# Performance work log

Measured on AMD Instinct MI355X. Metric: run time of the kernel, lower is better.

The kernel has to match this reference:

```python
import jax, jax.numpy as jnp
import numpy as np

D = 1024
N_HEADS = 16
D_HEAD = D // N_HEADS


def setup_inputs() -> dict:
    key = jax.random.key(0)
    ks = jax.random.split(key, 7)
    B, S = 4, 1024
    x = jax.random.normal(ks[0], (B, S, D), dtype=jnp.float32)
    # per-head linear params, stacked over heads: W[h] is [d_head, d_head] (torch Linear weight),
    # y = s @ W[h].T + b[h]
    scale = 1.0 / np.sqrt(D_HEAD)
    Wq = jax.random.uniform(ks[1], (N_HEADS, D_HEAD, D_HEAD), jnp.float32, -scale, scale)
    Wk = jax.random.uniform(ks[2], (N_HEADS, D_HEAD, D_HEAD), jnp.float32, -scale, scale)
    Wv = jax.random.uniform(ks[3], (N_HEADS, D_HEAD, D_HEAD), jnp.float32, -scale, scale)
    bq = jax.random.uniform(ks[4], (N_HEADS, D_HEAD), jnp.float32, -scale, scale)
    bk = jax.random.uniform(ks[5], (N_HEADS, D_HEAD), jnp.float32, -scale, scale)
    bv = jax.random.uniform(ks[6], (N_HEADS, D_HEAD), jnp.float32, -scale, scale)
    return {"pix_sequences": x, "Wq": Wq, "Wk": Wk, "Wv": Wv,
            "bq": bq, "bk": bk, "bv": bv}


def reference(pix_sequences, Wq, Wk, Wv, bq, bk, bv):
    B, S, d = pix_sequences.shape
    # split feature dim into heads: [B, S, H, dh]
    xh = pix_sequences.reshape(B, S, N_HEADS, D_HEAD)
    # per-head linear: y = s @ W.T + b
    q = jnp.einsum('bshd,hed->bshe', xh, Wq) + bq  # [B,S,H,dh]
    k = jnp.einsum('bshd,hed->bshe', xh, Wk) + bk
    v = jnp.einsum('bshd,hed->bshe', xh, Wv) + bv
    scores = jnp.einsum('bqhd,bkhd->bhqk', q, k) / jnp.sqrt(jnp.float32(D_HEAD))
    attn = jax.nn.softmax(scores, axis=-1)  # [B,H,S,S]
    out = jnp.einsum('bhqk,bkhd->bqhd', attn, v)  # [B,S,H,dh]
    return out.reshape(B, S, d)
```

## Files before the change

kernel.cpp:

```cpp
#include <hip/hip_runtime.h>
#include <hip/hip_bf16.h>

constexpr int BB = 4;
constexpr int SS = 1024;
constexpr int HH = 16;
constexpr int DH = 64;
constexpr int DM = 1024;

using f32x16 = __attribute__((ext_vector_type(16))) float;
using s16x8  = __attribute__((ext_vector_type(8))) short;

__device__ __forceinline__ f32x16 mfma32(s16x8 a, s16x8 b, f32x16 c) {
    return __builtin_amdgcn_mfma_f32_32x32x16_bf16(a, b, c, 0, 0, 0);
}

__device__ __forceinline__ unsigned short bf16bits(float x) {
    union { __hip_bfloat16 h; unsigned short s; } cv;
    cv.h = __float2bfloat16(x);
    return cv.s;
}
__device__ __forceinline__ unsigned pk_bf16(float lo, float hi) {
    return (unsigned)bf16bits(lo) | ((unsigned)bf16bits(hi) << 16);
}

__device__ __forceinline__ float fast_exp2(float x) {
#if __has_builtin(__builtin_amdgcn_exp2f)
    return __builtin_amdgcn_exp2f(x);
#else
    return __expf(x * 0.6931471805599453f);
#endif
}

__global__ __launch_bounds__(256) void qkv_proj_kernel(
    const float* __restrict__ x,
    const float* __restrict__ Wq, const float* __restrict__ Wk, const float* __restrict__ Wv,
    const float* __restrict__ bq, const float* __restrict__ bk, const float* __restrict__ bv,
    __hip_bfloat16* __restrict__ q_ws, __hip_bfloat16* __restrict__ k_ws,
    __hip_bfloat16* __restrict__ v_ws)
{
    const int bid  = blockIdx.x;
    const int tile = bid & 7;
    const int pair = bid >> 3;
    const int b = pair >> 4, h = pair & 15;
    const int t = threadIdx.x;
    const int w = t >> 6, l = t & 63;
    const int lq = l & 31, hi = l >> 5;
    const int s0 = tile * 128;

    __shared__ __align__(16) char Xs[16384];
    __shared__ __align__(16) char Kt[16384];
    __shared__ __align__(16) char Vt[16384];

    {
        const float* xb = x + (size_t)(b * SS + s0) * DM + h * DH;
        #pragma unroll
        for (int i = 0; i < 8; ++i) {
            const int c  = t + 256 * i;
            const int r  = c >> 4, cw = c & 15;
            float4 v4 = *reinterpret_cast<const float4*>(xb + (size_t)r * DM + cw * 4);
            uint2 p;
            p.x = pk_bf16(v4.x, v4.y);
            p.y = pk_bf16(v4.z, v4.w);
            *reinterpret_cast<uint2*>(Xs + r * 128 + ((cw * 8) ^ ((r & 7) << 4))) = p;
        }
    }
    __syncthreads();

    const int arow = w * 32 + lq;
    const int asw  = (arow & 7) << 4;
    s16x8 af[4];
    #pragma unroll
    for (int s = 0; s < 4; ++s)
        af[s] = *reinterpret_cast<const s16x8*>(Xs + arow * 128 + ((s * 32 + hi * 16) ^ asw));
    __syncthreads();

    #pragma unroll
    for (int m = 0; m < 3; ++m) {
        const float* Wm = (m == 0) ? Wq : (m == 1) ? Wk : Wv;
        const float* bm = (m == 0) ? bq : (m == 1) ? bk : bv;

        f32x16 a0, a1;
        #pragma unroll
        for (int r = 0; r < 16; ++r) { a0[r] = 0.0f; a1[r] = 0.0f; }

        #pragma unroll
        for (int s = 0; s < 4; ++s) {
            const float* wp0 = Wm + (size_t)(h * DH + lq) * DH + s * 16 + hi * 8;
            const float* wp1 = wp0 + 32 * DH;
            float4 wa0 = reinterpret_cast<const float4*>(wp0)[0];
            float4 wb0 = reinterpret_cast<const float4*>(wp0)[1];
            float4 wa1 = reinterpret_cast<const float4*>(wp1)[0];
            float4 wb1 = reinterpret_cast<const float4*>(wp1)[1];
            union { unsigned u[4]; s16x8 v; } bf0, bf1;
            bf0.u[0] = pk_bf16(wa0.x, wa0.y); bf0.u[1] = pk_bf16(wa0.z, wa0.w);
            bf0.u[2] = pk_bf16(wb0.x, wb0.y); bf0.u[3] = pk_bf16(wb0.z, wb0.w);
            bf1.u[0] = pk_bf16(wa1.x, wa1.y); bf1.u[1] = pk_bf16(wa1.z, wa1.w);
            bf1.u[2] = pk_bf16(wb1.x, wb1.y); bf1.u[3] = pk_bf16(wb1.z, wb1.w);
            a0 = mfma32(af[s], bf0.v, a0);
            a1 = mfma32(af[s], bf1.v, a1);
        }

        const float bias0 = bm[h * DH + lq];
        const float bias1 = bm[h * DH + 32 + lq];

        if (m < 2) {
            char* T = (m == 0) ? Xs : Kt;
            #pragma unroll
            for (int r = 0; r < 16; ++r) {
                const int row = w * 32 + (r & 3) + 8 * (r >> 2) + 4 * hi;
                const int sw  = (row & 7) << 4;
                *reinterpret_cast<unsigned short*>(T + row * 128 + ((lq * 2) ^ sw)) =
                    bf16bits(a0[r] + bias0);
                *reinterpret_cast<unsigned short*>(T + row * 128 + (((32 + lq) * 2) ^ sw)) =
                    bf16bits(a1[r] + bias1);
            }
        } else {
            #pragma unroll
            for (int g = 0; g < 4; ++g) {
                const int off = w * 64 + g * 16 + hi * 8;
                uint2 p0, p1;
                p0.x = pk_bf16(a0[4*g+0] + bias0, a0[4*g+1] + bias0);
                p0.y = pk_bf16(a0[4*g+2] + bias0, a0[4*g+3] + bias0);
                p1.x = pk_bf16(a1[4*g+0] + bias1, a1[4*g+1] + bias1);
                p1.y = pk_bf16(a1[4*g+2] + bias1, a1[4*g+3] + bias1);
                *reinterpret_cast<uint2*>(Vt + lq * 256 + (off ^ ((lq & 7) << 4))) = p0;
                *reinterpret_cast<uint2*>(Vt + (32 + lq) * 256 + (off ^ (((32 + lq) & 7) << 4))) = p1;
            }
        }
    }
    __syncthreads();

    #pragma unroll
    for (int i = 0; i < 4; ++i) {
        const int c   = t + 256 * i;
        const int row = c >> 3, cc = c & 7;
        const int off = row * 128 + ((cc * 16) ^ ((row & 7) << 4));
        s16x8 qv = *reinterpret_cast<const s16x8*>(Xs + off);
        *reinterpret_cast<s16x8*>(q_ws + ((size_t)pair * SS + s0 + row) * DH + cc * 8) = qv;
        s16x8 kv = *reinterpret_cast<const s16x8*>(Kt + off);
        *reinterpret_cast<s16x8*>(k_ws + ((size_t)pair * SS + s0 + row) * DH + cc * 8) = kv;
    }
    #pragma unroll
    for (int i = 0; i < 4; ++i) {
        const int c   = t + 256 * i;
        const int row = c >> 4, cc = c & 15;
        s16x8 vv = *reinterpret_cast<const s16x8*>(
            Vt + row * 256 + ((cc * 16) ^ ((row & 7) << 4)));
        *reinterpret_cast<s16x8*>(v_ws + ((size_t)pair * DH + row) * SS + s0 + cc * 8) = vv;
    }
}

__global__ __launch_bounds__(256) void attn_kernel(
    const __hip_bfloat16* __restrict__ q_ws,
    const __hip_bfloat16* __restrict__ k_ws,
    const __hip_bfloat16* __restrict__ v_ws,
    float* __restrict__ out)
{
    const int bid  = blockIdx.x;
    const int lbid = (bid & 7) * 64 + (bid >> 3);
    const int qt   = lbid & 7;
    const int pair = lbid >> 3;
    const int b = pair >> 4, h = pair & 15;
    const int t = threadIdx.x;
    const int w = t >> 6, l = t & 63;
    const int lq = l & 31, hi = l >> 5;

    __shared__ __align__(16) char Kl[2][8192];
    __shared__ __align__(16) char Vl[2][8192];

    const __hip_bfloat16* qp = q_ws + ((size_t)pair * SS + qt * 128 + w * 32 + lq) * DH + hi * 8;
    s16x8 qf[4];
    #pragma unroll
    for (int s5 = 0; s5 < 4; ++s5)
        qf[s5] = *reinterpret_cast<const s16x8*>(qp + s5 * 16);

    const int u0 = t, u1 = t + 256;
    const __hip_bfloat16* kb = k_ws + (size_t)pair * SS * DH;
    const __hip_bfloat16* vb = v_ws + (size_t)pair * DH * SS;
    const int ksw0 = (u0 ^ ((u0 >> 3) & 7)) * 16;
    const int ksw1 = (u1 ^ ((u1 >> 3) & 7)) * 16;
    const size_t voff0 = (size_t)(u0 >> 3) * SS + (u0 & 7) * 8;
    const size_t voff1 = (size_t)(u1 >> 3) * SS + (u1 & 7) * 8;

    {
        s16x8 k0 = *reinterpret_cast<const s16x8*>(kb + u0 * 8);
        s16x8 k1 = *reinterpret_cast<const s16x8*>(kb + u1 * 8);
        s16x8 v0 = *reinterpret_cast<const s16x8*>(vb + voff0);
        s16x8 v1 = *reinterpret_cast<const s16x8*>(vb + voff1);
        *reinterpret_cast<s16x8*>(Kl[0] + ksw0) = k0;
        *reinterpret_cast<s16x8*>(Kl[0] + ksw1) = k1;
        *reinterpret_cast<s16x8*>(Vl[0] + ksw0) = v0;
        *reinterpret_cast<s16x8*>(Vl[0] + ksw1) = v1;
    }
    __syncthreads();

    f32x16 o0, o1;
    #pragma unroll
    for (int r = 0; r < 16; ++r) { o0[r] = 0.0f; o1[r] = 0.0f; }
    float m_run = -3.0e38f, lsum = 0.0f;
    const float cml = 0.18033688011112042f;

    const int kbase0 = lq * 128;
    const int kbase1 = (32 + lq) * 128;
    const int swz = (lq & 7) << 4;

    int p = 0;
    s16x8 kr0, kr1, vr0, vr1;
    for (int kt = 0; kt < 16; ++kt) {
        if (kt < 15) {
            kr0 = *reinterpret_cast<const s16x8*>(kb + (kt + 1) * 4096 + u0 * 8);
            kr1 = *reinterpret_cast<const s16x8*>(kb + (kt + 1) * 4096 + u1 * 8);
            vr0 = *reinterpret_cast<const s16x8*>(vb + voff0 + (kt + 1) * 64);
            vr1 = *reinterpret_cast<const s16x8*>(vb + voff1 + (kt + 1) * 64);
        }
        const char* Kp = Kl[p];
        const char* Vp = Vl[p];

        f32x16 sc0, sc1;
        #pragma unroll
        for (int r = 0; r < 16; ++r) { sc0[r] = 0.0f; sc1[r] = 0.0f; }
        #pragma unroll
        for (int s5 = 0; s5 < 4; ++s5) {
            const int co = (2 * s5 + hi) << 4;
            s16x8 ka = *reinterpret_cast<const s16x8*>(Kp + kbase0 + (co ^ swz));
            sc0 = mfma32(ka, qf[s5], sc0);
        }
        #pragma unroll
        for (int s5 = 0; s5 < 4; ++s5) {
            const int co = (2 * s5 + hi) << 4;
            s16x8 ka = *reinterpret_cast<const s16x8*>(Kp + kbase1 + (co ^ swz));
            sc1 = mfma32(ka, qf[s5], sc1);
        }

        float tm[16];
        #pragma unroll
        for (int r = 0; r < 16; ++r) tm[r] = fmaxf(sc0[r], sc1[r]);
        #pragma unroll
        for (int s = 8; s >= 1; s >>= 1)
            #pragma unroll
            for (int r = 0; r < 8; ++r)
                if (r < s) tm[r] = fmaxf(tm[r], tm[r + s]);
        float mx = fmaxf(tm[0], __shfl_xor(tm[0], 32));

        if (!__all((mx - m_run) * cml <= 8.0f)) {
            float mnew  = fmaxf(m_run, mx);
            float alpha = fast_exp2((m_run - mnew) * cml);
            lsum *= alpha;
            #pragma unroll
            for (int r = 0; r < 16; ++r) { o0[r] *= alpha; o1[r] *= alpha; }
            m_run = mnew;
        }
        const float nm = -m_run * cml;
        float ts[16];
        #pragma unroll
        for (int r = 0; r < 16; ++r) {
            sc0[r] = fast_exp2(fmaf(sc0[r], cml, nm));
            sc1[r] = fast_exp2(fmaf(sc1[r], cml, nm));
            ts[r]  = sc0[r] + sc1[r];
        }
        #pragma unroll
        for (int s = 8; s >= 1; s >>= 1)
            #pragma unroll
            for (int r = 0; r < 8; ++r)
                if (r < s) ts[r] += ts[r + s];
        lsum += ts[0] + __shfl_xor(ts[0], 32);

        #pragma unroll
        for (int s5 = 0; s5 < 4; ++s5) {
            const int sb8 = (s5 & 1) * 8;
            unsigned a0, b0, a1, b1;
            if (s5 < 2) {
                a0 = pk_bf16(sc0[sb8 + 0], sc0[sb8 + 1]);
                b0 = pk_bf16(sc0[sb8 + 4], sc0[sb8 + 5]);
                a1 = pk_bf16(sc0[sb8 + 2], sc0[sb8 + 3]);
                b1 = pk_bf16(sc0[sb8 + 6], sc0[sb8 + 7]);
            } else {
                a0 = pk_bf16(sc1[sb8 + 0], sc1[sb8 + 1]);
                b0 = pk_bf16(sc1[sb8 + 4], sc1[sb8 + 5]);
                a1 = pk_bf16(sc1[sb8 + 2], sc1[sb8 + 3]);
                b1 = pk_bf16(sc1[sb8 + 6], sc1[sb8 + 7]);
            }
            const unsigned sa0 = (unsigned)__shfl_xor((int)a0, 32);
            const unsigned sb0 = (unsigned)__shfl_xor((int)b0, 32);
            const unsigned sa1 = (unsigned)__shfl_xor((int)a1, 32);
            const unsigned sb1 = (unsigned)__shfl_xor((int)b1, 32);
            union { unsigned u[4]; s16x8 v; } afr;
            afr.u[0] = hi ? sb0 : a0;
            afr.u[1] = hi ? sb1 : a1;
            afr.u[2] = hi ? b0 : sa0;
            afr.u[3] = hi ? b1 : sa1;
            const int co = (2 * s5 + hi) << 4;
            s16x8 vb0 = *reinterpret_cast<const s16x8*>(Vp + kbase0 + (co ^ swz));
            o0 = mfma32(afr.v, vb0, o0);
            s16x8 vb1 = *reinterpret_cast<const s16x8*>(Vp + kbase1 + (co ^ swz));
            o1 = mfma32(afr.v, vb1, o1);
        }

        if (kt < 15) {
            *reinterpret_cast<s16x8*>(Kl[p ^ 1] + ksw0) = kr0;
            *reinterpret_cast<s16x8*>(Kl[p ^ 1] + ksw1) = kr1;
            *reinterpret_cast<s16x8*>(Vl[p ^ 1] + ksw0) = vr0;
            *reinterpret_cast<s16x8*>(Vl[p ^ 1] + ksw1) = vr1;
        }
        __syncthreads();
        p ^= 1;
    }

    const float inv = 1.0f / lsum;
    #pragma unroll
    for (int r = 0; r < 16; ++r) {
        const int qr = (r & 3) + 8 * (r >> 2) + 4 * hi;
        const float invr = __shfl(inv, qr);
        float* op = out + ((size_t)b * SS + qt * 128 + w * 32 + qr) * DM + h * DH + lq;
        op[0]  = o0[r] * invr;
        op[32] = o1[r] * invr;
    }
}

extern "C" void kernel_launch(void* const* d_in, const int* in_sizes, int n_in,
                              void* d_out, int out_size, void* d_ws, size_t ws_size,
                              hipStream_t stream) {
    const float* x  = (const float*)d_in[0];
    const float* Wq = (const float*)d_in[1];
    const float* Wk = (const float*)d_in[2];
    const float* Wv = (const float*)d_in[3];
    const float* bq = (const float*)d_in[4];
    const float* bk = (const float*)d_in[5];
    const float* bv = (const float*)d_in[6];
    float* out = (float*)d_out;

    __hip_bfloat16* q_ws = (__hip_bfloat16*)d_ws;
    __hip_bfloat16* k_ws = q_ws + (size_t)BB * HH * SS * DH;
    __hip_bfloat16* v_ws = k_ws + (size_t)BB * HH * SS * DH;

    qkv_proj_kernel<<<dim3(BB * HH * (SS / 128)), dim3(256), 0, stream>>>(
        x, Wq, Wk, Wv, bq, bk, bv, q_ws, k_ws, v_ws);
    attn_kernel<<<dim3(BB * HH * (SS / 64 / 2)), dim3(256), 0, stream>>>(
        q_ws, k_ws, v_ws, out);
}
```

Measured before the change: 60.02 us.

## Split KV range across two warp groups per block and merge softmax partials

```diff
diff --git a/kernel.cpp b/kernel.cpp
--- a/kernel.cpp
+++ b/kernel.cpp
@@ -150,7 +150,7 @@
     }
 }
 
-__global__ __launch_bounds__(256) void attn_kernel(
+__global__ __launch_bounds__(512, 4) void attn_kernel(
     const __hip_bfloat16* __restrict__ q_ws,
     const __hip_bfloat16* __restrict__ k_ws,
     const __hip_bfloat16* __restrict__ v_ws,
@@ -164,33 +164,36 @@
     const int t = threadIdx.x;
     const int w = t >> 6, l = t & 63;
     const int lq = l & 31, hi = l >> 5;
-
-    __shared__ __align__(16) char Kl[2][8192];
-    __shared__ __align__(16) char Vl[2][8192];
-
-    const __hip_bfloat16* qp = q_ws + ((size_t)pair * SS + qt * 128 + w * 32 + lq) * DH + hi * 8;
+    const int qg = w & 3, p = w >> 2;
+
+    __shared__ __align__(16) char smem[65536];
+
+    const __hip_bfloat16* qp =
+        q_ws + ((size_t)pair * SS + qt * 128 + qg * 32 + lq) * DH + hi * 8;
     s16x8 qf[4];
     #pragma unroll
     for (int s5 = 0; s5 < 4; ++s5)
         qf[s5] = *reinterpret_cast<const s16x8*>(qp + s5 * 16);
 
-    const int u0 = t, u1 = t + 256;
+    const int u0 = t, u1 = t + 512;
     const __hip_bfloat16* kb = k_ws + (size_t)pair * SS * DH;
     const __hip_bfloat16* vb = v_ws + (size_t)pair * DH * SS;
-    const int ksw0 = (u0 ^ ((u0 >> 3) & 7)) * 16;
-    const int ksw1 = (u1 ^ ((u1 >> 3) & 7)) * 16;
-    const size_t voff0 = (size_t)(u0 >> 3) * SS + (u0 & 7) * 8;
-    const size_t voff1 = (size_t)(u1 >> 3) * SS + (u1 & 7) * 8;
+    const int kOff0 = (u0 ^ ((u0 >> 3) & 7)) * 16;
+    const int kOff1 = (u1 ^ ((u1 >> 3) & 7)) * 16;
+    const int vOff0 = (u0 >> 4) * 256 + (((u0 & 15) ^ ((u0 >> 4) & 15)) << 4);
+    const int vOff1 = (u1 >> 4) * 256 + (((u1 & 15) ^ ((u1 >> 4) & 15)) << 4);
+    const size_t vs0 = (size_t)(u0 >> 4) * SS + (u0 & 15) * 8;
+    const size_t vs1 = (size_t)(u1 >> 4) * SS + (u1 & 15) * 8;
 
     {
         s16x8 k0 = *reinterpret_cast<const s16x8*>(kb + u0 * 8);
         s16x8 k1 = *reinterpret_cast<const s16x8*>(kb + u1 * 8);
-        s16x8 v0 = *reinterpret_cast<const s16x8*>(vb + voff0);
-        s16x8 v1 = *reinterpret_cast<const s16x8*>(vb + voff1);
-        *reinterpret_cast<s16x8*>(Kl[0] + ksw0) = k0;
-        *reinterpret_cast<s16x8*>(Kl[0] + ksw1) = k1;
-        *reinterpret_cast<s16x8*>(Vl[0] + ksw0) = v0;
-        *reinterpret_cast<s16x8*>(Vl[0] + ksw1) = v1;
+        s16x8 v0 = *reinterpret_cast<const s16x8*>(vb + vs0);
+        s16x8 v1 = *reinterpret_cast<const s16x8*>(vb + vs1);
+        *reinterpret_cast<s16x8*>(smem + kOff0) = k0;
+        *reinterpret_cast<s16x8*>(smem + kOff1) = k1;
+        *reinterpret_cast<s16x8*>(smem + 16384 + vOff0) = v0;
+        *reinterpret_cast<s16x8*>(smem + 16384 + vOff1) = v1;
     }
     __syncthreads();
 
@@ -200,21 +203,23 @@
     float m_run = -3.0e38f, lsum = 0.0f;
     const float cml = 0.18033688011112042f;
 
-    const int kbase0 = lq * 128;
-    const int kbase1 = (32 + lq) * 128;
-    const int swz = (lq & 7) << 4;
-
-    int p = 0;
+    const int kbase0 = (p * 64 + lq) * 128;
+    const int kbase1 = kbase0 + 32 * 128;
+    const int swzK = (lq & 7) << 4;
+    const int swzV = (lq & 15) << 4;
+    const int vrow0 = lq * 256, vrow1 = (32 + lq) * 256;
+
+    int bufp = 0;
     s16x8 kr0, kr1, vr0, vr1;
-    for (int kt = 0; kt < 16; ++kt) {
-        if (kt < 15) {
-            kr0 = *reinterpret_cast<const s16x8*>(kb + (kt + 1) * 4096 + u0 * 8);
-            kr1 = *reinterpret_cast<const s16x8*>(kb + (kt + 1) * 4096 + u1 * 8);
-            vr0 = *reinterpret_cast<const s16x8*>(vb + voff0 + (kt + 1) * 64);
-            vr1 = *reinterpret_cast<const s16x8*>(vb + voff1 + (kt + 1) * 64);
-        }
-        const char* Kp = Kl[p];
-        const char* Vp = Vl[p];
+    for (int st = 0; st < 8; ++st) {
+        if (st < 7) {
+            kr0 = *reinterpret_cast<const s16x8*>(kb + (st + 1) * 8192 + u0 * 8);
+            kr1 = *reinterpret_cast<const s16x8*>(kb + (st + 1) * 8192 + u1 * 8);
+            vr0 = *reinterpret_cast<const s16x8*>(vb + vs0 + (st + 1) * 128);
+            vr1 = *reinterpret_cast<const s16x8*>(vb + vs1 + (st + 1) * 128);
+        }
+        const char* Kp = smem + bufp * 32768;
+        const char* Vp = Kp + 16384;
 
         f32x16 sc0, sc1;
         #pragma unroll
@@ -222,13 +227,13 @@
         #pragma unroll
         for (int s5 = 0; s5 < 4; ++s5) {
             const int co = (2 * s5 + hi) << 4;
-            s16x8 ka = *reinterpret_cast<const s16x8*>(Kp + kbase0 + (co ^ swz));
+            s16x8 ka = *reinterpret_cast<const s16x8*>(Kp + kbase0 + (co ^ swzK));
             sc0 = mfma32(ka, qf[s5], sc0);
         }
         #pragma unroll
         for (int s5 = 0; s5 < 4; ++s5) {
             const int co = (2 * s5 + hi) << 4;
-            s16x8 ka = *reinterpret_cast<const s16x8*>(Kp + kbase1 + (co ^ swz));
+            s16x8 ka = *reinterpret_cast<const s16x8*>(Kp + kbase1 + (co ^ swzK));
             sc1 = mfma32(ka, qf[s5], sc1);
         }
 
@@ -290,30 +295,53 @@
             afr.u[2] = hi ? b0 : sa0;
             afr.u[3] = hi ? b1 : sa1;
             const int co = (2 * s5 + hi) << 4;
-            s16x8 vb0 = *reinterpret_cast<const s16x8*>(Vp + kbase0 + (co ^ swz));
+            s16x8 vb0 = *reinterpret_cast<const s16x8*>(Vp + vrow0 + ((p * 128 + co) ^ swzV));
             o0 = mfma32(afr.v, vb0, o0);
-            s16x8 vb1 = *reinterpret_cast<const s16x8*>(Vp + kbase1 + (co ^ swz));
+            s16x8 vb1 = *reinterpret_cast<const s16x8*>(Vp + vrow1 + ((p * 128 + co) ^ swzV));
             o1 = mfma32(afr.v, vb1, o1);
         }
 
-        if (kt < 15) {
-            *reinterpret_cast<s16x8*>(Kl[p ^ 1] + ksw0) = kr0;
-            *reinterpret_cast<s16x8*>(Kl[p ^ 1] + ksw1) = kr1;
-            *reinterpret_cast<s16x8*>(Vl[p ^ 1] + ksw0) = vr0;
-            *reinterpret_cast<s16x8*>(Vl[p ^ 1] + ksw1) = vr1;
+        if (st < 7) {
+            char* Kn = smem + (bufp ^ 1) * 32768;
+            *reinterpret_cast<s16x8*>(Kn + kOff0) = kr0;
+            *reinterpret_cast<s16x8*>(Kn + kOff1) = kr1;
+            *reinterpret_cast<s16x8*>(Kn + 16384 + vOff0) = vr0;
+            *reinterpret_cast<s16x8*>(Kn + 16384 + vOff1) = vr1;
         }
         __syncthreads();
-        p ^= 1;
-    }
-
-    const float inv = 1.0f / lsum;
-    #pragma unroll
-    for (int r = 0; r < 16; ++r) {
-        const int qr = (r & 3) + 8 * (r >> 2) + 4 * hi;
-        const float invr = __shfl(inv, qr);
-        float* op = out + ((size_t)b * SS + qt * 128 + w * 32 + qr) * DM + h * DH + lq;
-        op[0]  = o0[r] * invr;
-        op[32] = o1[r] * invr;
+        bufp ^= 1;
+    }
+
+    float* Obuf = reinterpret_cast<float*>(smem + qg * 8192);
+    float* mlb  = reinterpret_cast<float*>(smem + 32768 + qg * 256);
+    if (p == 1) {
+        #pragma unroll
+        for (int r = 0; r < 16; ++r) {
+            const int qr = (r & 3) + 8 * (r >> 2) + 4 * hi;
+            Obuf[qr * 64 + lq]      = o0[r];
+            Obuf[qr * 64 + 32 + lq] = o1[r];
+        }
+        mlb[lq]      = m_run;
+        mlb[32 + lq] = lsum;
+    }
+    __syncthreads();
+    if (p == 0) {
+        const float m1 = mlb[lq];
+        const float l1 = mlb[32 + lq];
+        const float M  = fmaxf(m_run, m1);
+        const float e0 = fast_exp2((m_run - M) * cml);
+        const float e1 = fast_exp2((m1 - M) * cml);
+        const float inv = 1.0f / fmaf(lsum, e0, l1 * e1);
+        const float f0 = e0 * inv, f1 = e1 * inv;
+        #pragma unroll
+        for (int r = 0; r < 16; ++r) {
+            const int qr = (r & 3) + 8 * (r >> 2) + 4 * hi;
+            const float f0r = __shfl(f0, qr);
+            const float f1r = __shfl(f1, qr);
+            float* op = out + ((size_t)b * SS + qt * 128 + qg * 32 + qr) * DM + h * DH + lq;
+            op[0]  = o0[r] * f0r + Obuf[qr * 64 + lq]      * f1r;
+            op[32] = o1[r] * f0r + Obuf[qr * 64 + 32 + lq] * f1r;
+        }
     }
 }
 
@@ -335,6 +363,6 @@
 
     qkv_proj_kernel<<<dim3(BB * HH * (SS / 128)), dim3(256), 0, stream>>>(
         x, Wq, Wk, Wv, bq, bk, bv, q_ws, k_ws, v_ws);
-    attn_kernel<<<dim3(BB * HH * (SS / 64 / 2)), dim3(256), 0, stream>>>(
+    attn_kernel<<<dim3(BB * HH * (SS / 128)), dim3(512), 0, stream>>>(
         q_ws, k_ws, v_ws, out);
 }
```

Measured after the change: 61.39 us. 2.3% more time.

## Split attention KV range across waves with in-block LSE merge

Applied to the files above, without the earlier changes.

```diff
diff --git a/kernel.cpp b/kernel.cpp
--- a/kernel.cpp
+++ b/kernel.cpp
@@ -29,6 +29,11 @@
 #else
     return __expf(x * 0.6931471805599453f);
 #endif
+}
+
+__device__ __forceinline__ int kperm(int g) {
+    const int m = g & 12;
+    return (m == 4 || m == 8) ? (g ^ 12) : g;
 }
 
 __global__ __launch_bounds__(256) void qkv_proj_kernel(
@@ -150,49 +155,32 @@
     }
 }
 
-__global__ __launch_bounds__(256) void attn_kernel(
+__global__ __launch_bounds__(256, 4) void attn_kernel(
     const __hip_bfloat16* __restrict__ q_ws,
     const __hip_bfloat16* __restrict__ k_ws,
     const __hip_bfloat16* __restrict__ v_ws,
     float* __restrict__ out)
 {
     const int bid  = blockIdx.x;
-    const int lbid = (bid & 7) * 64 + (bid >> 3);
-    const int qt   = lbid & 7;
-    const int pair = lbid >> 3;
+    const int lbid = (bid & 7) * 256 + (bid >> 3);
+    const int qg   = lbid & 31;
+    const int pair = lbid >> 5;
     const int b = pair >> 4, h = pair & 15;
     const int t = threadIdx.x;
-    const int w = t >> 6, l = t & 63;
+    const int p = t >> 6, l = t & 63;
     const int lq = l & 31, hi = l >> 5;
 
-    __shared__ __align__(16) char Kl[2][8192];
-    __shared__ __align__(16) char Vl[2][8192];
-
-    const __hip_bfloat16* qp = q_ws + ((size_t)pair * SS + qt * 128 + w * 32 + lq) * DH + hi * 8;
+    __shared__ __align__(16) char smem[16896];
+
+    const __hip_bfloat16* qp = q_ws + ((size_t)pair * SS + qg * 32 + lq) * DH + hi * 8;
     s16x8 qf[4];
     #pragma unroll
     for (int s5 = 0; s5 < 4; ++s5)
         qf[s5] = *reinterpret_cast<const s16x8*>(qp + s5 * 16);
 
-    const int u0 = t, u1 = t + 256;
-    const __hip_bfloat16* kb = k_ws + (size_t)pair * SS * DH;
-    const __hip_bfloat16* vb = v_ws + (size_t)pair * DH * SS;
-    const int ksw0 = (u0 ^ ((u0 >> 3) & 7)) * 16;
-    const int ksw1 = (u1 ^ ((u1 >> 3) & 7)) * 16;
-    const size_t voff0 = (size_t)(u0 >> 3) * SS + (u0 & 7) * 8;
-    const size_t voff1 = (size_t)(u1 >> 3) * SS + (u1 & 7) * 8;
-
-    {
-        s16x8 k0 = *reinterpret_cast<const s16x8*>(kb + u0 * 8);
-        s16x8 k1 = *reinterpret_cast<const s16x8*>(kb + u1 * 8);
-        s16x8 v0 = *reinterpret_cast<const s16x8*>(vb + voff0);
-        s16x8 v1 = *reinterpret_cast<const s16x8*>(vb + voff1);
-        *reinterpret_cast<s16x8*>(Kl[0] + ksw0) = k0;
-        *reinterpret_cast<s16x8*>(Kl[0] + ksw1) = k1;
-        *reinterpret_cast<s16x8*>(Vl[0] + ksw0) = v0;
-        *reinterpret_cast<s16x8*>(Vl[0] + ksw1) = v1;
-    }
-    __syncthreads();
+    const __hip_bfloat16* kp  = k_ws + ((size_t)pair * SS + kperm(lq)) * DH + hi * 8;
+    const __hip_bfloat16* vp0 = v_ws + ((size_t)pair * DH + lq) * SS + hi * 8;
+    const __hip_bfloat16* vp1 = vp0 + (size_t)32 * SS;
 
     f32x16 o0, o1;
     #pragma unroll
@@ -200,41 +188,22 @@
     float m_run = -3.0e38f, lsum = 0.0f;
     const float cml = 0.18033688011112042f;
 
-    const int kbase0 = lq * 128;
-    const int kbase1 = (32 + lq) * 128;
-    const int swz = (lq & 7) << 4;
-
-    int p = 0;
-    s16x8 kr0, kr1, vr0, vr1;
-    for (int kt = 0; kt < 16; ++kt) {
-        if (kt < 15) {
-            kr0 = *reinterpret_cast<const s16x8*>(kb + (kt + 1) * 4096 + u0 * 8);
-            kr1 = *reinterpret_cast<const s16x8*>(kb + (kt + 1) * 4096 + u1 * 8);
-            vr0 = *reinterpret_cast<const s16x8*>(vb + voff0 + (kt + 1) * 64);
-            vr1 = *reinterpret_cast<const s16x8*>(vb + voff1 + (kt + 1) * 64);
-        }
-        const char* Kp = Kl[p];
-        const char* Vp = Vl[p];
-
-        f32x16 sc0, sc1;
-        #pragma unroll
-        for (int r = 0; r < 16; ++r) { sc0[r] = 0.0f; sc1[r] = 0.0f; }
-        #pragma unroll
-        for (int s5 = 0; s5 < 4; ++s5) {
-            const int co = (2 * s5 + hi) << 4;
-            s16x8 ka = *reinterpret_cast<const s16x8*>(Kp + kbase0 + (co ^ swz));
-            sc0 = mfma32(ka, qf[s5], sc0);
-        }
-        #pragma unroll
-        for (int s5 = 0; s5 < 4; ++s5) {
-            const int co = (2 * s5 + hi) << 4;
-            s16x8 ka = *reinterpret_cast<const s16x8*>(Kp + kbase1 + (co ^ swz));
-            sc1 = mfma32(ka, qf[s5], sc1);
-        }
+    for (int g8 = 0; g8 < 8; ++g8) {
+        const int g = p * 8 + g8;
+        const __hip_bfloat16* kg  = kp  + (size_t)g * 32 * DH;
+        const __hip_bfloat16* vg0 = vp0 + g * 32;
+        const __hip_bfloat16* vg1 = vp1 + g * 32;
+
+        f32x16 sc;
+        #pragma unroll
+        for (int r = 0; r < 16; ++r) sc[r] = 0.0f;
+        #pragma unroll
+        for (int s5 = 0; s5 < 4; ++s5)
+            sc = mfma32(*reinterpret_cast<const s16x8*>(kg + s5 * 16), qf[s5], sc);
 
         float tm[16];
         #pragma unroll
-        for (int r = 0; r < 16; ++r) tm[r] = fmaxf(sc0[r], sc1[r]);
+        for (int r = 0; r < 16; ++r) tm[r] = sc[r];
         #pragma unroll
         for (int s = 8; s >= 1; s >>= 1)
             #pragma unroll
@@ -247,16 +216,19 @@
             float alpha = fast_exp2((m_run - mnew) * cml);
             lsum *= alpha;
             #pragma unroll
-            for (int r = 0; r < 16; ++r) { o0[r] *= alpha; o1[r] *= alpha; }
+            for (int r = 0; r < 16; ++r) {
+                const int qr = (r & 3) + 8 * (r >> 2) + 4 * hi;
+                const float ar = __shfl(alpha, qr);
+                o0[r] *= ar; o1[r] *= ar;
+            }
             m_run = mnew;
         }
         const float nm = -m_run * cml;
         float ts[16];
         #pragma unroll
         for (int r = 0; r < 16; ++r) {
-            sc0[r] = fast_exp2(fmaf(sc0[r], cml, nm));
-            sc1[r] = fast_exp2(fmaf(sc1[r], cml, nm));
-            ts[r]  = sc0[r] + sc1[r];
+            sc[r] = fast_exp2(fmaf(sc[r], cml, nm));
+            ts[r] = sc[r];
         }
         #pragma unroll
         for (int s = 8; s >= 1; s >>= 1)
@@ -265,55 +237,84 @@
                 if (r < s) ts[r] += ts[r + s];
         lsum += ts[0] + __shfl_xor(ts[0], 32);
 
-        #pragma unroll
-        for (int s5 = 0; s5 < 4; ++s5) {
-            const int sb8 = (s5 & 1) * 8;
-            unsigned a0, b0, a1, b1;
-            if (s5 < 2) {
-                a0 = pk_bf16(sc0[sb8 + 0], sc0[sb8 + 1]);
-                b0 = pk_bf16(sc0[sb8 + 4], sc0[sb8 + 5]);
-                a1 = pk_bf16(sc0[sb8 + 2], sc0[sb8 + 3]);
-                b1 = pk_bf16(sc0[sb8 + 6], sc0[sb8 + 7]);
-            } else {
-                a0 = pk_bf16(sc1[sb8 + 0], sc1[sb8 + 1]);
-                b0 = pk_bf16(sc1[sb8 + 4], sc1[sb8 + 5]);
-                a1 = pk_bf16(sc1[sb8 + 2], sc1[sb8 + 3]);
-                b1 = pk_bf16(sc1[sb8 + 6], sc1[sb8 + 7]);
-            }
-            const unsigned sa0 = (unsigned)__shfl_xor((int)a0, 32);
-            const unsigned sb0 = (unsigned)__shfl_xor((int)b0, 32);
-            const unsigned sa1 = (unsigned)__shfl_xor((int)a1, 32);
-            const unsigned sb1 = (unsigned)__shfl_xor((int)b1, 32);
-            union { unsigned u[4]; s16x8 v; } afr;
-            afr.u[0] = hi ? sb0 : a0;
-            afr.u[1] = hi ? sb1 : a1;
-            afr.u[2] = hi ? b0 : sa0;
-            afr.u[3] = hi ? b1 : sa1;
-            const int co = (2 * s5 + hi) << 4;
-            s16x8 vb0 = *reinterpret_cast<const s16x8*>(Vp + kbase0 + (co ^ swz));
-            o0 = mfma32(afr.v, vb0, o0);
-            s16x8 vb1 = *reinterpret_cast<const s16x8*>(Vp + kbase1 + (co ^ swz));
-            o1 = mfma32(afr.v, vb1, o1);
-        }
-
-        if (kt < 15) {
-            *reinterpret_cast<s16x8*>(Kl[p ^ 1] + ksw0) = kr0;
-            *reinterpret_cast<s16x8*>(Kl[p ^ 1] + ksw1) = kr1;
-            *reinterpret_cast<s16x8*>(Vl[p ^ 1] + ksw0) = vr0;
-            *reinterpret_cast<s16x8*>(Vl[p ^ 1] + ksw1) = vr1;
-        }
-        __syncthreads();
-        p ^= 1;
-    }
-
-    const float inv = 1.0f / lsum;
-    #pragma unroll
-    for (int r = 0; r < 16; ++r) {
-        const int qr = (r & 3) + 8 * (r >> 2) + 4 * hi;
-        const float invr = __shfl(inv, qr);
-        float* op = out + ((size_t)b * SS + qt * 128 + w * 32 + qr) * DM + h * DH + lq;
-        op[0]  = o0[r] * invr;
-        op[32] = o1[r] * invr;
+        union { unsigned u[4]; s16x8 v; } af0, af1;
+        af0.u[0] = pk_bf16(sc[0], sc[1]);   af0.u[1] = pk_bf16(sc[2], sc[3]);
+        af0.u[2] = pk_bf16(sc[4], sc[5]);   af0.u[3] = pk_bf16(sc[6], sc[7]);
+        af1.u[0] = pk_bf16(sc[8], sc[9]);   af1.u[1] = pk_bf16(sc[10], sc[11]);
+        af1.u[2] = pk_bf16(sc[12], sc[13]); af1.u[3] = pk_bf16(sc[14], sc[15]);
+
+        s16x8 v00 = *reinterpret_cast<const s16x8*>(vg0);
+        s16x8 v01 = *reinterpret_cast<const s16x8*>(vg0 + 16);
+        s16x8 v10 = *reinterpret_cast<const s16x8*>(vg1);
+        s16x8 v11 = *reinterpret_cast<const s16x8*>(vg1 + 16);
+        o0 = mfma32(af0.v, v00, o0);
+        o0 = mfma32(af1.v, v01, o0);
+        o1 = mfma32(af0.v, v10, o1);
+        o1 = mfma32(af1.v, v11, o1);
+    }
+
+    float* O0 = reinterpret_cast<float*>(smem);
+    float* M0 = reinterpret_cast<float*>(smem + 8192);
+    float* O1 = reinterpret_cast<float*>(smem + 8448);
+    float* M1 = reinterpret_cast<float*>(smem + 16640);
+
+    if (p == 1 || p == 3) {
+        float* O = (p == 1) ? O0 : O1;
+        float* M = (p == 1) ? M0 : M1;
+        #pragma unroll
+        for (int r = 0; r < 16; ++r) {
+            const int qr = (r & 3) + 8 * (r >> 2) + 4 * hi;
+            O[qr * 64 + lq]      = o0[r];
+            O[qr * 64 + 32 + lq] = o1[r];
+        }
+        if (hi == 0) { M[lq] = m_run; M[32 + lq] = lsum; }
+    }
+    __syncthreads();
+    if (p == 0 || p == 2) {
+        float* O = (p == 0) ? O0 : O1;
+        float* M = (p == 0) ? M0 : M1;
+        const float m1 = M[lq], l1 = M[32 + lq];
+        const float Mx = fmaxf(m_run, m1);
+        const float e0 = fast_exp2((m_run - Mx) * cml);
+        const float e1 = fast_exp2((m1 - Mx) * cml);
+        #pragma unroll
+        for (int r = 0; r < 16; ++r) {
+            const int qr = (r & 3) + 8 * (r >> 2) + 4 * hi;
+            const float e0r = __shfl(e0, qr);
+            const float e1r = __shfl(e1, qr);
+            o0[r] = o0[r] * e0r + O[qr * 64 + lq] * e1r;
+            o1[r] = o1[r] * e0r + O[qr * 64 + 32 + lq] * e1r;
+        }
+        lsum = lsum * e0 + l1 * e1;
+        m_run = Mx;
+    }
+    __syncthreads();
+    if (p == 2) {
+        #pragma unroll
+        for (int r = 0; r < 16; ++r) {
+            const int qr = (r & 3) + 8 * (r >> 2) + 4 * hi;
+            O1[qr * 64 + lq]      = o0[r];
+            O1[qr * 64 + 32 + lq] = o1[r];
+        }
+        if (hi == 0) { M1[lq] = m_run; M1[32 + lq] = lsum; }
+    }
+    __syncthreads();
+    if (p == 0) {
+        const float m1 = M1[lq], l1 = M1[32 + lq];
+        const float Mx = fmaxf(m_run, m1);
+        const float e0 = fast_exp2((m_run - Mx) * cml);
+        const float e1 = fast_exp2((m1 - Mx) * cml);
+        const float inv = 1.0f / (lsum * e0 + l1 * e1);
+        const float f0 = e0 * inv, f1 = e1 * inv;
+        #pragma unroll
+        for (int r = 0; r < 16; ++r) {
+            const int qr = (r & 3) + 8 * (r >> 2) + 4 * hi;
+            const float f0r = __shfl(f0, qr);
+            const float f1r = __shfl(f1, qr);
+            float* op = out + ((size_t)b * SS + qg * 32 + qr) * DM + h * DH + lq;
+            op[0]  = o0[r] * f0r + O1[qr * 64 + lq]      * f1r;
+            op[32] = o1[r] * f0r + O1[qr * 64 + 32 + lq] * f1r;
+        }
     }
 }
 
@@ -335,6 +336,6 @@
 
     qkv_proj_kernel<<<dim3(BB * HH * (SS / 128)), dim3(256), 0, stream>>>(
         x, Wq, Wk, Wv, bq, bk, bv, q_ws, k_ws, v_ws);
-    attn_kernel<<<dim3(BB * HH * (SS / 64 / 2)), dim3(256), 0, stream>>>(
+    attn_kernel<<<dim3(BB * HH * (SS / 32)), dim3(256), 0, stream>>>(
         q_ws, k_ws, v_ws, out);
 }
```

After: 92.42 us. +54.0%, slower.
